# Optimization experiments

Hardware: AMD Instinct MI355X
Metric: run time of the kernel (lower is better)

The kernel has to match this reference:

```python
import jax, jax.numpy as jnp
import numpy as np

N_NODES = 100000
N_EDGES = 1000000
D_IN, D_HID, D_OUT = 128, 128, 64
EPS = 1e-5


def setup_inputs() -> dict:
    key = jax.random.key(0)
    ks = jax.random.split(key, 10)
    x = jax.random.normal(ks[0], (N_NODES, D_IN), dtype=jnp.float32)
    edge_index = jax.random.randint(ks[1], (2, N_EDGES), 0, N_NODES, dtype=jnp.int64)
    # GCNConv weights (glorot-ish scale) and biases
    W0 = jax.random.normal(ks[2], (D_IN, D_HID), dtype=jnp.float32) / np.sqrt(D_IN)
    b0 = jnp.zeros((D_HID,), dtype=jnp.float32)
    W1 = jax.random.normal(ks[3], (D_HID, D_HID), dtype=jnp.float32) / np.sqrt(D_HID)
    b1 = jnp.zeros((D_HID,), dtype=jnp.float32)
    W2 = jax.random.normal(ks[4], (D_HID, D_OUT), dtype=jnp.float32) / np.sqrt(D_HID)
    b2 = jnp.zeros((D_OUT,), dtype=jnp.float32)
    # LayerNorm params for the n_layer-1 = 2 norm layers
    g0 = jnp.ones((D_HID,), dtype=jnp.float32)
    bn0 = jnp.zeros((D_HID,), dtype=jnp.float32)
    g1 = jnp.ones((D_HID,), dtype=jnp.float32)
    bn1 = jnp.zeros((D_HID,), dtype=jnp.float32)
    return {"x": x, "edge_index": edge_index, "W0": W0, "b0": b0,
            "W1": W1, "b1": b1, "W2": W2, "b2": b2,
            "g0": g0, "bn0": bn0, "g1": g1, "bn1": bn1}


def _gcn_norm(edge_index, n_nodes):
    # add self-loops, compute symmetric normalization deg^-1/2 * deg^-1/2
    loop = jnp.arange(n_nodes, dtype=edge_index.dtype)
    src = jnp.concatenate([edge_index[0], loop])
    dst = jnp.concatenate([edge_index[1], loop])
    deg = jax.ops.segment_sum(jnp.ones_like(dst, dtype=jnp.float32), dst,
                              num_segments=n_nodes)
    dinv = jnp.where(deg > 0, jax.lax.rsqrt(deg), 0.0)
    coef = dinv[src] * dinv[dst]  # [E + N]
    return src, dst, coef


def _gcn_conv(x, W, b, src, dst, coef, n_nodes):
    h = x @ W                              # [N, out]
    msg = h[src] * coef[:, None]           # gather + scale, [E+N, out]
    agg = jax.ops.segment_sum(msg, dst, num_segments=n_nodes)
    return agg + b


def _layer_norm(h, g, b):
    mu = jnp.mean(h, axis=-1, keepdims=True)
    var = jnp.mean(jnp.square(h - mu), axis=-1, keepdims=True)
    return (h - mu) * jax.lax.rsqrt(var + EPS) * g + b


def reference(x, edge_index, W0, b0, W1, b1, W2, b2, g0, bn0, g1, bn1):
    n = x.shape[0]
    src, dst, coef = _gcn_norm(edge_index, n)
    h = _gcn_conv(x, W0, b0, src, dst, coef, n)
    # layer 1 -> 2 (dropout is identity in eval mode)
    h = jax.nn.relu(_layer_norm(h, g0, bn0))
    h = _gcn_conv(h, W1, b1, src, dst, coef, n)
    # layer 2 -> 3
    h = jax.nn.relu(_layer_norm(h, g1, bn1))
    h = _gcn_conv(h, W2, b2, src, dst, coef, n)
    return h
```

## Files before the change

### kernel.cpp

```cpp
#include <hip/hip_runtime.h>
#include <hip/hip_bf16.h>
#include <stdint.h>

#define EPS 1e-5f
#define KPAD 136
#define NB 256
#define BSH 9

typedef __attribute__((ext_vector_type(4))) float f32x4;
typedef _Float16 f16;
typedef __attribute__((ext_vector_type(2))) _Float16 f16x2;
typedef __attribute__((ext_vector_type(8))) _Float16 f16x8;

__device__ __forceinline__ int rfl(int x) { return __builtin_amdgcn_readfirstlane(x); }
__device__ __forceinline__ float rflf(float x) {
    return __int_as_float(__builtin_amdgcn_readfirstlane(__float_as_int(x)));
}

__device__ __forceinline__ bool detect64(const uint32_t* w) {
    int lane = threadIdx.x & 63;
    uint32_t odd = w[1 + 2 * lane] | w[129 + 2 * lane];
    return !__any(odd != 0u);
}

__global__ __launch_bounds__(256) void k_scatter(const void* __restrict__ eidx,
                                                 int* __restrict__ bcount,
                                                 int2* __restrict__ bpairs,
                                                 int E, int cap) {
    __shared__ int hist[NB];
    __shared__ int base[NB];
    bool is64 = detect64((const uint32_t*)eidx);
    int t = threadIdx.x;
    if (t < NB) hist[t] = 0;
    __syncthreads();
    int e0 = blockIdx.x * 1024 + t * 4;
    int s[4], d[4], b[4], rank[4];
    #pragma unroll
    for (int i = 0; i < 4; i++) {
        int e = e0 + i;
        if (e < E) {
            if (is64) {
                const long long* p = (const long long*)eidx;
                s[i] = (int)p[e];
                d[i] = (int)p[(size_t)E + e];
            } else {
                const int* p = (const int*)eidx;
                s[i] = p[e];
                d[i] = p[(size_t)E + e];
            }
            b[i] = d[i] >> BSH;
            rank[i] = atomicAdd(&hist[b[i]], 1);
        }
    }
    __syncthreads();
    if (t < NB) base[t] = hist[t] ? atomicAdd(&bcount[t], hist[t]) : 0;
    __syncthreads();
    #pragma unroll
    for (int i = 0; i < 4; i++) {
        int e = e0 + i;
        if (e < E) {
            int idx = base[b[i]] + rank[i];
            if (idx < cap) bpairs[(size_t)b[i] * cap + idx] = make_int2(s[i], d[i]);
        }
    }
}

__global__ void k_bscan(const int* __restrict__ bcount, int* __restrict__ bbase, int used) {
    int lane = threadIdx.x;
    int carry = 0;
    for (int base = 0; base < used; base += 64) {
        int i = base + lane;
        int v = (i < used) ? bcount[i] : 0;
        int orig = v;
        #pragma unroll
        for (int off = 1; off < 64; off <<= 1) {
            int t = __shfl_up(v, off);
            if (lane >= off) v += t;
        }
        if (i < used) bbase[i] = carry + v - orig;
        carry += __shfl(v, 63);
    }
}

__global__ __launch_bounds__(256) void k_fill3(const int2* __restrict__ bpairs,
                                               const int* __restrict__ bcount,
                                               const int* __restrict__ bbase,
                                               int* __restrict__ rowptr,
                                               float* __restrict__ dinv,
                                               int* __restrict__ adj,
                                               int N, int E, int cap) {
    __shared__ int hist[512];
    __shared__ int wsum[4];
    __shared__ int wexcl[4];
    int b = blockIdx.x;
    int t = threadIdx.x;
    int lane = t & 63;
    int wv = t >> 6;
    int d0 = b << BSH;
    int W = N - d0;
    if (W > 512) W = 512;
    int n = bcount[b];
    if (n > cap) n = cap;
    int base = bbase[b];
    const int2* p = bpairs + (size_t)b * cap;

    hist[t] = 0;
    hist[t + 256] = 0;
    __syncthreads();
    for (int i = t; i < n; i += 256) atomicAdd(&hist[p[i].y - d0], 1);
    __syncthreads();
    int i0 = 2 * t, i1 = 2 * t + 1;
    int a = hist[i0], bv = hist[i1];
    int s2 = a + bv;
    int incl = s2;
    #pragma unroll
    for (int off = 1; off < 64; off <<= 1) {
        int tv = __shfl_up(incl, off);
        if (lane >= off) incl += tv;
    }
    if (lane == 63) wsum[wv] = incl;
    __syncthreads();
    if (t == 0) {
        int r = 0;
        #pragma unroll
        for (int i = 0; i < 4; i++) { wexcl[i] = r; r += wsum[i]; }
    }
    __syncthreads();
    int excl = incl - s2 + wexcl[wv];
    if (i0 < W) {
        rowptr[d0 + i0] = base + excl;
        dinv[d0 + i0] = rsqrtf((float)(a + 1));
    }
    if (i1 < W) {
        rowptr[d0 + i1] = base + excl + a;
        dinv[d0 + i1] = rsqrtf((float)(bv + 1));
    }
    if (b == gridDim.x - 1 && t == 0) rowptr[N] = E;
    __syncthreads();
    hist[i0] = excl;
    hist[i1] = excl + a;
    __syncthreads();
    for (int i = t; i < n; i += 256) {
        int2 pr = p[i];
        int pos = atomicAdd(&hist[pr.y - d0], 1);
        adj[base + pos] = pr.x;
    }
}

__global__ void k_wconv(const float* __restrict__ W0, const float* __restrict__ W1,
                        const float* __restrict__ W2, f16* __restrict__ T0,
                        f16* __restrict__ T1, f16* __restrict__ T2) {
    int layer = blockIdx.y;
    const float* W = layer == 0 ? W0 : (layer == 1 ? W1 : W2);
    f16* T = layer == 0 ? T0 : (layer == 1 ? T1 : T2);
    int outc = (layer == 2) ? 64 : 128;
    int tid = blockIdx.x * 256 + threadIdx.x;
    if (tid >= 128 * outc) return;
    int k = tid / outc, c = tid % outc;
    float f = W[tid];
    f16 hb = (f16)f;
    f16 lb = (f16)(f - (float)hb);
    T[c * KPAD + k] = hb;
    T[outc * KPAD + c * KPAD + k] = lb;
}

template <int OUTC, typename AT>
__global__ __launch_bounds__(256, OUTC == 64 ? 4 : 2)
void k_gemm_mfma(const AT* __restrict__ A, const f16* __restrict__ WT,
                 const float* __restrict__ dinv, f16* __restrict__ C, int N) {
    __shared__ f16 lds[2 * OUTC * KPAD];
    const int t = threadIdx.x;
    const int n16 = (2 * OUTC * KPAD * 2) / 16;
    for (int i = t; i < n16; i += 256)
        ((float4*)lds)[i] = ((const float4*)WT)[i];

    const int lane = t & 63;
    const int wv = t >> 6;
    const int c = lane & 15;
    const int hq = lane >> 4;
    const int rowbase = blockIdx.x * 128 + wv * 32;

    constexpr bool IS16 = (sizeof(AT) == 2);
    f16x8 ahi[2][4], alo[2][4];
    #pragma unroll
    for (int rt = 0; rt < 2; ++rt) {
        int ar = rowbase + rt * 16 + c;
        if (ar > N - 1) ar = N - 1;
        const AT* ap = A + (size_t)ar * 128 + hq * 8;
        #pragma unroll
        for (int ks = 0; ks < 4; ++ks) {
            if constexpr (IS16) {
                ahi[rt][ks] = *(const f16x8*)(ap + ks * 32);
            } else {
                float4 p = *(const float4*)(ap + ks * 32);
                float4 q = *(const float4*)(ap + ks * 32 + 4);
                float v[8] = {p.x, p.y, p.z, p.w, q.x, q.y, q.z, q.w};
                #pragma unroll
                for (int j = 0; j < 8; ++j) {
                    f16 hb = (f16)v[j];
                    ahi[rt][ks][j] = hb;
                    alo[rt][ks][j] = (f16)(v[j] - (float)hb);
                }
            }
        }
    }
    float di[2][4];
    #pragma unroll
    for (int rt = 0; rt < 2; ++rt)
        #pragma unroll
        for (int r = 0; r < 4; ++r) {
            int row = rowbase + rt * 16 + hq * 4 + r;
            di[rt][r] = (row < N) ? dinv[row] : 0.f;
        }
    __syncthreads();

    #pragma unroll
    for (int ct = 0; ct < OUTC / 16; ++ct) {
        const f16* bp = &lds[(ct * 16 + c) * KPAD + hq * 8];
        f16x8 bhi[4], blo[4];
        #pragma unroll
        for (int ks = 0; ks < 4; ++ks) {
            bhi[ks] = *reinterpret_cast<const f16x8*>(bp + ks * 32);
            blo[ks] = *reinterpret_cast<const f16x8*>(bp + OUTC * KPAD + ks * 32);
        }
        f32x4 acc0 = {0.f, 0.f, 0.f, 0.f};
        f32x4 acc1 = {0.f, 0.f, 0.f, 0.f};
        #pragma unroll
        for (int ks = 0; ks < 4; ++ks) {
            acc0 = __builtin_amdgcn_mfma_f32_16x16x32_f16(ahi[0][ks], bhi[ks], acc0, 0, 0, 0);
            acc1 = __builtin_amdgcn_mfma_f32_16x16x32_f16(ahi[1][ks], bhi[ks], acc1, 0, 0, 0);
            if constexpr (!IS16) {
                acc0 = __builtin_amdgcn_mfma_f32_16x16x32_f16(alo[0][ks], bhi[ks], acc0, 0, 0, 0);
                acc1 = __builtin_amdgcn_mfma_f32_16x16x32_f16(alo[1][ks], bhi[ks], acc1, 0, 0, 0);
            }
            acc0 = __builtin_amdgcn_mfma_f32_16x16x32_f16(ahi[0][ks], blo[ks], acc0, 0, 0, 0);
            acc1 = __builtin_amdgcn_mfma_f32_16x16x32_f16(ahi[1][ks], blo[ks], acc1, 0, 0, 0);
        }
        const int col = ct * 16 + c;
        #pragma unroll
        for (int rt = 0; rt < 2; ++rt) {
            f32x4 a = rt ? acc1 : acc0;
            int row0 = rowbase + rt * 16 + hq * 4;
            #pragma unroll
            for (int r = 0; r < 4; ++r) {
                int row = row0 + r;
                if (row < N) C[(size_t)row * OUTC + col] = (f16)(a[r] * di[rt][r]);
            }
        }
    }
}

__global__ __launch_bounds__(256) void k_agg_ln(const f16* __restrict__ h,
                                                const int* __restrict__ rowptr,
                                                const int* __restrict__ adj,
                                                const float* __restrict__ dinv,
                                                const float* __restrict__ bias,
                                                const float* __restrict__ g,
                                                const float* __restrict__ bn,
                                                f16* __restrict__ out, int N) {
    int lane = threadIdx.x & 63;
    int v = rfl(blockIdx.x * 4 + (threadIdx.x >> 6));
    if (v >= N) return;
    int c = lane * 2;
    float dv = rflf(dinv[v]);
    f16x2 hv = *(const f16x2*)&h[(size_t)v * 128 + c];
    float ax = (float)hv[0];
    float ay = (float)hv[1];
    int e0 = rfl(rowptr[v]);
    int e1 = rfl(rowptr[v + 1]);
    int e = e0;
    for (; e + 16 <= e1; e += 16) {
        const f16* rp[16];
        #pragma unroll
        for (int i = 0; i < 16; i++) rp[i] = h + (size_t)rfl(adj[e + i]) * 128;
        f16x2 hh[16];
        #pragma unroll
        for (int i = 0; i < 16; i++) hh[i] = *(const f16x2*)&rp[i][c];
        #pragma unroll
        for (int i = 0; i < 16; i++) { ax += (float)hh[i][0]; ay += (float)hh[i][1]; }
    }
    for (; e + 4 <= e1; e += 4) {
        const f16* rp[4];
        #pragma unroll
        for (int i = 0; i < 4; i++) rp[i] = h + (size_t)rfl(adj[e + i]) * 128;
        f16x2 hh[4];
        #pragma unroll
        for (int i = 0; i < 4; i++) hh[i] = *(const f16x2*)&rp[i][c];
        #pragma unroll
        for (int i = 0; i < 4; i++) { ax += (float)hh[i][0]; ay += (float)hh[i][1]; }
    }
    for (; e < e1; e++) {
        const f16* rp = h + (size_t)rfl(adj[e]) * 128;
        f16x2 hu = *(const f16x2*)&rp[c];
        ax += (float)hu[0];
        ay += (float)hu[1];
    }
    float2 bb = *(const float2*)&bias[c];
    float px = fmaf(dv, ax, bb.x);
    float py = fmaf(dv, ay, bb.y);
    float s = px + py;
    #pragma unroll
    for (int m = 32; m >= 1; m >>= 1) s += __shfl_xor(s, m);
    float mu = s * (1.0f / 128.0f);
    float dx = px - mu, dy = py - mu;
    float vs = dx * dx + dy * dy;
    #pragma unroll
    for (int m = 32; m >= 1; m >>= 1) vs += __shfl_xor(vs, m);
    float rs = rsqrtf(vs * (1.0f / 128.0f) + EPS);
    float2 gg = *(const float2*)&g[c];
    float2 bnv = *(const float2*)&bn[c];
    float ox = fmaxf(dx * rs * gg.x + bnv.x, 0.0f);
    float oy = fmaxf(dy * rs * gg.y + bnv.y, 0.0f);
    f16x2 o;
    o[0] = (f16)ox;
    o[1] = (f16)oy;
    *(f16x2*)&out[(size_t)v * 128 + c] = o;
}

__global__ __launch_bounds__(256) void k_agg_out(const f16* __restrict__ h,
                                                 const int* __restrict__ rowptr,
                                                 const int* __restrict__ adj,
                                                 const float* __restrict__ dinv,
                                                 const float* __restrict__ bias,
                                                 float* __restrict__ out, int N) {
    int lane = threadIdx.x & 63;
    int v = rfl(blockIdx.x * 4 + (threadIdx.x >> 6));
    if (v >= N) return;
    float dv = rflf(dinv[v]);
    float acc = (float)h[(size_t)v * 64 + lane];
    int e0 = rfl(rowptr[v]);
    int e1 = rfl(rowptr[v + 1]);
    int e = e0;
    for (; e + 16 <= e1; e += 16) {
        const f16* rp[16];
        #pragma unroll
        for (int i = 0; i < 16; i++) rp[i] = h + (size_t)rfl(adj[e + i]) * 64;
        f16 hh[16];
        #pragma unroll
        for (int i = 0; i < 16; i++) hh[i] = rp[i][lane];
        #pragma unroll
        for (int i = 0; i < 16; i++) acc += (float)hh[i];
    }
    for (; e + 4 <= e1; e += 4) {
        const f16* rp[4];
        #pragma unroll
        for (int i = 0; i < 4; i++) rp[i] = h + (size_t)rfl(adj[e + i]) * 64;
        f16 hh[4];
        #pragma unroll
        for (int i = 0; i < 4; i++) hh[i] = rp[i][lane];
        #pragma unroll
        for (int i = 0; i < 4; i++) acc += (float)hh[i];
    }
    for (; e < e1; e++) {
        acc += (float)h[(size_t)rfl(adj[e]) * 64 + lane];
    }
    out[(size_t)v * 64 + lane] = fmaf(dv, acc, bias[lane]);
}

extern "C" void kernel_launch(void* const* d_in, const int* in_sizes, int n_in,
                              void* d_out, int out_size, void* d_ws, size_t ws_size,
                              hipStream_t stream) {
    const float* x    = (const float*)d_in[0];
    const void*  eidx = d_in[1];
    const float* W0 = (const float*)d_in[2];
    const float* b0 = (const float*)d_in[3];
    const float* W1 = (const float*)d_in[4];
    const float* b1 = (const float*)d_in[5];
    const float* W2 = (const float*)d_in[6];
    const float* b2 = (const float*)d_in[7];
    const float* g0 = (const float*)d_in[8];
    const float* bn0 = (const float*)d_in[9];
    const float* g1 = (const float*)d_in[10];
    const float* bn1 = (const float*)d_in[11];

    int N = in_sizes[0] / 128;
    int E = in_sizes[1] / 2;

    int used = ((N - 1) >> BSH) + 1;
    int cap = (E / used) * 2 + 256;

    char* p = (char*)d_ws;
    auto alloc = [&](size_t bytes) {
        char* r = p;
        p += (bytes + 255) & ~(size_t)255;
        return r;
    };
    int*   rowptr  = (int*)alloc(((size_t)N + 1) * 4);
    float* dinv    = (float*)alloc((size_t)N * 4);
    int*   adj     = (int*)alloc((size_t)E * 4);
    int2*  bpairs  = (int2*)alloc((size_t)used * cap * 8);
    int*   bcount  = (int*)alloc(NB * 4);
    int*   bbase   = (int*)alloc(NB * 4);
    f16*   wt0     = (f16*)alloc(2 * 128 * KPAD * 2);
    f16*   wt1     = (f16*)alloc(2 * 128 * KPAD * 2);
    f16*   wt2     = (f16*)alloc(2 * 64 * KPAD * 2);
    f16*   bufA    = (f16*)alloc((size_t)N * 128 * 2);
    f16*   bufB    = (f16*)alloc((size_t)N * 128 * 2);

    int sb = (E + 1023) / 1024;

    hipMemsetAsync(bcount, 0, NB * 4, stream);
    k_wconv<<<dim3(64, 3), 256, 0, stream>>>(W0, W1, W2, wt0, wt1, wt2);
    k_scatter<<<sb, 256, 0, stream>>>(eidx, bcount, bpairs, E, cap);
    k_bscan<<<1, 64, 0, stream>>>(bcount, bbase, used);
    k_fill3<<<used, 256, 0, stream>>>(bpairs, bcount, bbase, rowptr, dinv, adj, N, E, cap);

    int gemmb = (N + 127) / 128;
    int aggb = (N + 3) / 4;

    k_gemm_mfma<128, float><<<gemmb, 256, 0, stream>>>(x, wt0, dinv, bufA, N);
    k_agg_ln<<<aggb, 256, 0, stream>>>(bufA, rowptr, adj, dinv, b0, g0, bn0, bufB, N);
    k_gemm_mfma<128, f16><<<gemmb, 256, 0, stream>>>(bufB, wt1, dinv, bufA, N);
    k_agg_ln<<<aggb, 256, 0, stream>>>(bufA, rowptr, adj, dinv, b1, g1, bn1, bufB, N);
    k_gemm_mfma<64, f16><<<gemmb, 256, 0, stream>>>(bufB, wt2, dinv, bufA, N);
    k_agg_out<<<aggb, 256, 0, stream>>>(bufA, rowptr, adj, dinv, b2, (float*)d_out, N);
}
```

Before: 261.9 us.

## Replace global-atomic bucket scatter with block-local sorted staging and per-bucket gather

The CSR build no longer reserves bucket slots through global atomics and scattered int2 writes. Each block now sorts its 4096 edges by destination bucket in shared memory, writes them out contiguously as packed 32-bit words (local dst in the high bits, src in the low 23 bits), and records per-block bucket counts and offsets. k_fill3 scans those per-block counts and binary-searches them to gather its bucket's edges. This removes the global atomics, halves the staging footprint, and drops the capacity cap, but adds a binary search per edge in both fill passes and a serial k_bsum loop over about 245 blocks. The 23-bit packing limits source indices to under 2^23, and MAXBLK caps E at about 8M.

Result: slower. 295.6 us (+12.9%).

```diff
diff --git a/kernel.cpp b/kernel.cpp
--- a/kernel.cpp
+++ b/kernel.cpp
@@ -6,6 +6,8 @@
 #define KPAD 136
 #define NB 256
 #define BSH 9
+#define EB 4096
+#define MAXBLK 2048
 
 typedef __attribute__((ext_vector_type(4))) float f32x4;
 typedef _Float16 f16;
@@ -24,19 +26,22 @@
 }
 
 __global__ __launch_bounds__(256) void k_scatter(const void* __restrict__ eidx,
-                                                 int* __restrict__ bcount,
-                                                 int2* __restrict__ bpairs,
-                                                 int E, int cap) {
+                                                 uint32_t* __restrict__ staged,
+                                                 int* __restrict__ cntmat,
+                                                 int* __restrict__ offmat, int E) {
+    __shared__ uint32_t sst[EB];
     __shared__ int hist[NB];
-    __shared__ int base[NB];
+    __shared__ int off[NB];
+    __shared__ int cur[NB];
+    __shared__ int wsum[4], wexcl[4];
     bool is64 = detect64((const uint32_t*)eidx);
-    int t = threadIdx.x;
-    if (t < NB) hist[t] = 0;
-    __syncthreads();
-    int e0 = blockIdx.x * 1024 + t * 4;
-    int s[4], d[4], b[4], rank[4];
-    #pragma unroll
-    for (int i = 0; i < 4; i++) {
+    int t = threadIdx.x, lane = t & 63, wv = t >> 6;
+    hist[t] = 0;
+    __syncthreads();
+    int e0 = blockIdx.x * EB + t * 16;
+    int s[16], d[16];
+    #pragma unroll
+    for (int i = 0; i < 16; i++) {
         int e = e0 + i;
         if (e < E) {
             if (is64) {
@@ -48,75 +53,138 @@
                 s[i] = p[e];
                 d[i] = p[(size_t)E + e];
             }
-            b[i] = d[i] >> BSH;
-            rank[i] = atomicAdd(&hist[b[i]], 1);
-        }
-    }
-    __syncthreads();
-    if (t < NB) base[t] = hist[t] ? atomicAdd(&bcount[t], hist[t]) : 0;
-    __syncthreads();
-    #pragma unroll
-    for (int i = 0; i < 4; i++) {
+            atomicAdd(&hist[d[i] >> BSH], 1);
+        }
+    }
+    __syncthreads();
+    int v = hist[t];
+    int incl = v;
+    #pragma unroll
+    for (int o = 1; o < 64; o <<= 1) {
+        int tv = __shfl_up(incl, o);
+        if (lane >= o) incl += tv;
+    }
+    if (lane == 63) wsum[wv] = incl;
+    __syncthreads();
+    if (t == 0) {
+        int r = 0;
+        #pragma unroll
+        for (int i = 0; i < 4; i++) { wexcl[i] = r; r += wsum[i]; }
+    }
+    __syncthreads();
+    int ex = incl - v + wexcl[wv];
+    off[t] = ex;
+    cur[t] = ex;
+    __syncthreads();
+    #pragma unroll
+    for (int i = 0; i < 16; i++) {
         int e = e0 + i;
         if (e < E) {
-            int idx = base[b[i]] + rank[i];
-            if (idx < cap) bpairs[(size_t)b[i] * cap + idx] = make_int2(s[i], d[i]);
-        }
-    }
-}
-
-__global__ void k_bscan(const int* __restrict__ bcount, int* __restrict__ bbase, int used) {
-    int lane = threadIdx.x;
-    int carry = 0;
-    for (int base = 0; base < used; base += 64) {
-        int i = base + lane;
-        int v = (i < used) ? bcount[i] : 0;
-        int orig = v;
-        #pragma unroll
-        for (int off = 1; off < 64; off <<= 1) {
-            int t = __shfl_up(v, off);
-            if (lane >= off) v += t;
-        }
-        if (i < used) bbase[i] = carry + v - orig;
-        carry += __shfl(v, 63);
-    }
-}
-
-__global__ __launch_bounds__(256) void k_fill3(const int2* __restrict__ bpairs,
-                                               const int* __restrict__ bcount,
+            int b = d[i] >> BSH;
+            int pos = atomicAdd(&cur[b], 1);
+            sst[pos] = ((uint32_t)(d[i] - (b << BSH)) << 23) | (uint32_t)s[i];
+        }
+    }
+    __syncthreads();
+    int tot = E - blockIdx.x * EB;
+    if (tot > EB) tot = EB;
+    uint32_t* gp = staged + (size_t)blockIdx.x * EB;
+    for (int i = t; i < tot; i += 256) gp[i] = sst[i];
+    cntmat[blockIdx.x * NB + t] = hist[t];
+    offmat[blockIdx.x * NB + t] = off[t];
+}
+
+__global__ __launch_bounds__(256) void k_bsum(const int* __restrict__ cntmat,
+                                              int* __restrict__ bbase, int nblk) {
+    __shared__ int wsum[4], wexcl[4];
+    int t = threadIdx.x, lane = t & 63, wv = t >> 6;
+    int s = 0;
+    for (int k = 0; k < nblk; k++) s += cntmat[k * NB + t];
+    int incl = s;
+    #pragma unroll
+    for (int o = 1; o < 64; o <<= 1) {
+        int tv = __shfl_up(incl, o);
+        if (lane >= o) incl += tv;
+    }
+    if (lane == 63) wsum[wv] = incl;
+    __syncthreads();
+    if (t == 0) {
+        int r = 0;
+        #pragma unroll
+        for (int i = 0; i < 4; i++) { wexcl[i] = r; r += wsum[i]; }
+    }
+    __syncthreads();
+    bbase[t] = incl - s + wexcl[wv];
+}
+
+__global__ __launch_bounds__(256) void k_fill3(const uint32_t* __restrict__ staged,
+                                               const int* __restrict__ cntmat,
+                                               const int* __restrict__ offmat,
                                                const int* __restrict__ bbase,
                                                int* __restrict__ rowptr,
                                                float* __restrict__ dinv,
                                                int* __restrict__ adj,
-                                               int N, int E, int cap) {
+                                               int N, int E, int nblk) {
+    __shared__ int segstart[MAXBLK + 1];
+    __shared__ int offk[MAXBLK];
     __shared__ int hist[512];
-    __shared__ int wsum[4];
-    __shared__ int wexcl[4];
-    int b = blockIdx.x;
-    int t = threadIdx.x;
-    int lane = t & 63;
-    int wv = t >> 6;
+    __shared__ int wsum[4], wexcl[4];
+    int b = blockIdx.x, t = threadIdx.x, lane = t & 63, wv = t >> 6;
     int d0 = b << BSH;
     int W = N - d0;
     if (W > 512) W = 512;
-    int n = bcount[b];
-    if (n > cap) n = cap;
-    int base = bbase[b];
-    const int2* p = bpairs + (size_t)b * cap;
-
+
+    int carry = 0;
+    for (int cb = 0; cb < nblk; cb += 256) {
+        int k = cb + t;
+        int v = (k < nblk) ? cntmat[k * NB + b] : 0;
+        int ok = (k < nblk) ? offmat[k * NB + b] : 0;
+        int incl = v;
+        #pragma unroll
+        for (int o = 1; o < 64; o <<= 1) {
+            int tv = __shfl_up(incl, o);
+            if (lane >= o) incl += tv;
+        }
+        if (lane == 63) wsum[wv] = incl;
+        __syncthreads();
+        if (t == 0) {
+            int r = 0;
+            #pragma unroll
+            for (int i = 0; i < 4; i++) { wexcl[i] = r; r += wsum[i]; }
+        }
+        __syncthreads();
+        if (k < nblk) {
+            segstart[k] = carry + incl - v + wexcl[wv];
+            offk[k] = ok;
+        }
+        carry += wsum[0] + wsum[1] + wsum[2] + wsum[3];
+        __syncthreads();
+    }
+    if (t == 0) segstart[nblk] = carry;
     hist[t] = 0;
     hist[t + 256] = 0;
     __syncthreads();
-    for (int i = t; i < n; i += 256) atomicAdd(&hist[p[i].y - d0], 1);
+    int n = segstart[nblk];
+    int base = bbase[b];
+
+    for (int i = t; i < n; i += 256) {
+        int lo = 0, hi = nblk;
+        while (hi - lo > 1) {
+            int mid = (lo + hi) >> 1;
+            if (segstart[mid] <= i) lo = mid; else hi = mid;
+        }
+        uint32_t u = staged[(size_t)lo * EB + offk[lo] + (i - segstart[lo])];
+        atomicAdd(&hist[u >> 23], 1);
+    }
     __syncthreads();
     int i0 = 2 * t, i1 = 2 * t + 1;
     int a = hist[i0], bv = hist[i1];
     int s2 = a + bv;
     int incl = s2;
     #pragma unroll
-    for (int off = 1; off < 64; off <<= 1) {
-        int tv = __shfl_up(incl, off);
-        if (lane >= off) incl += tv;
+    for (int o = 1; o < 64; o <<= 1) {
+        int tv = __shfl_up(incl, o);
+        if (lane >= o) incl += tv;
     }
     if (lane == 63) wsum[wv] = incl;
     __syncthreads();
@@ -141,9 +209,14 @@
     hist[i1] = excl + a;
     __syncthreads();
     for (int i = t; i < n; i += 256) {
-        int2 pr = p[i];
-        int pos = atomicAdd(&hist[pr.y - d0], 1);
-        adj[base + pos] = pr.x;
+        int lo = 0, hi = nblk;
+        while (hi - lo > 1) {
+            int mid = (lo + hi) >> 1;
+            if (segstart[mid] <= i) lo = mid; else hi = mid;
+        }
+        uint32_t u = staged[(size_t)lo * EB + offk[lo] + (i - segstart[lo])];
+        int pos = atomicAdd(&hist[u >> 23], 1);
+        adj[base + pos] = (int)(u & 0x7fffffu);
     }
 }
 
@@ -377,7 +450,7 @@
     int E = in_sizes[1] / 2;
 
     int used = ((N - 1) >> BSH) + 1;
-    int cap = (E / used) * 2 + 256;
+    int nblk = (E + EB - 1) / EB;
 
     char* p = (char*)d_ws;
     auto alloc = [&](size_t bytes) {
@@ -385,25 +458,23 @@
         p += (bytes + 255) & ~(size_t)255;
         return r;
     };
-    int*   rowptr  = (int*)alloc(((size_t)N + 1) * 4);
-    float* dinv    = (float*)alloc((size_t)N * 4);
-    int*   adj     = (int*)alloc((size_t)E * 4);
-    int2*  bpairs  = (int2*)alloc((size_t)used * cap * 8);
-    int*   bcount  = (int*)alloc(NB * 4);
-    int*   bbase   = (int*)alloc(NB * 4);
-    f16*   wt0     = (f16*)alloc(2 * 128 * KPAD * 2);
-    f16*   wt1     = (f16*)alloc(2 * 128 * KPAD * 2);
-    f16*   wt2     = (f16*)alloc(2 * 64 * KPAD * 2);
-    f16*   bufA    = (f16*)alloc((size_t)N * 128 * 2);
-    f16*   bufB    = (f16*)alloc((size_t)N * 128 * 2);
-
-    int sb = (E + 1023) / 1024;
-
-    hipMemsetAsync(bcount, 0, NB * 4, stream);
+    int*      rowptr = (int*)alloc(((size_t)N + 1) * 4);
+    float*    dinv   = (float*)alloc((size_t)N * 4);
+    int*      adj    = (int*)alloc((size_t)E * 4);
+    uint32_t* staged = (uint32_t*)alloc((size_t)nblk * EB * 4);
+    int*      cntmat = (int*)alloc((size_t)nblk * NB * 4);
+    int*      offmat = (int*)alloc((size_t)nblk * NB * 4);
+    int*      bbase  = (int*)alloc(NB * 4);
+    f16*      wt0    = (f16*)alloc(2 * 128 * KPAD * 2);
+    f16*      wt1    = (f16*)alloc(2 * 128 * KPAD * 2);
+    f16*      wt2    = (f16*)alloc(2 * 64 * KPAD * 2);
+    f16*      bufA   = (f16*)alloc((size_t)N * 128 * 2);
+    f16*      bufB   = (f16*)alloc((size_t)N * 128 * 2);
+
     k_wconv<<<dim3(64, 3), 256, 0, stream>>>(W0, W1, W2, wt0, wt1, wt2);
-    k_scatter<<<sb, 256, 0, stream>>>(eidx, bcount, bpairs, E, cap);
-    k_bscan<<<1, 64, 0, stream>>>(bcount, bbase, used);
-    k_fill3<<<used, 256, 0, stream>>>(bpairs, bcount, bbase, rowptr, dinv, adj, N, E, cap);
+    k_scatter<<<nblk, 256, 0, stream>>>(eidx, staged, cntmat, offmat, E);
+    k_bsum<<<1, 256, 0, stream>>>(cntmat, bbase, nblk);
+    k_fill3<<<used, 256, 0, stream>>>(staged, cntmat, offmat, bbase, rowptr, dinv, adj, N, E, nblk);
 
     int gemmb = (N + 127) / 128;
     int aggb = (N + 3) / 4;
```
